# Optimization experiments

Measured on AMD Instinct MI355X. Metric: run time of the kernel, lower is better.

The kernel has to match this reference:

```python
import jax, jax.numpy as jnp
import numpy as np
import math

# Model dims (see shape_source)
BATCH, SEQ, HH, WW = 32, 128, 32, 32   # x: (B, seq_len, H, W); L = H*W = 1024
D_MODEL = 1024                          # hidden_dim
N2 = 4                                  # n=8 -> 4 complex S4D modes
L_MAX = 64                              # SSM kernel length (l_max)


def _layernorm(x, gamma, beta, eps=1e-5):
    mu = jnp.mean(x, axis=-1, keepdims=True)
    var = jnp.var(x, axis=-1, keepdims=True)
    return (x - mu) * jax.lax.rsqrt(var + eps) * gamma + beta


def setup_inputs() -> dict:
    key = jax.random.key(0)
    ks = jax.random.split(key, 12)
    d_in = SEQ  # d_input = d_output = seq_len
    inp = {
        "x": jax.random.normal(ks[0], (BATCH, SEQ, HH, WW), dtype=jnp.float32),
        # encoder Linear(d_input -> d_model)
        "W_enc": jax.random.normal(ks[1], (d_in, D_MODEL), dtype=jnp.float32) / math.sqrt(d_in),
        "b_enc": jnp.zeros((D_MODEL,), dtype=jnp.float32),
        # S4D SSM parameters (per d_model channel, N2 complex modes)
        "log_dt": (jax.random.uniform(ks[2], (D_MODEL,), dtype=jnp.float32)
                   * (math.log(0.1) - math.log(0.001)) + math.log(0.001)),
        "A_log_real": jnp.full((D_MODEL, N2), math.log(0.5), dtype=jnp.float32),
        "A_imag": jnp.broadcast_to(math.pi * jnp.arange(N2, dtype=jnp.float32), (D_MODEL, N2)).copy(),
        "C_real": jax.random.normal(ks[3], (D_MODEL, N2), dtype=jnp.float32) * 0.5,
        "C_imag": jax.random.normal(ks[4], (D_MODEL, N2), dtype=jnp.float32) * 0.5,
        "D": jax.random.normal(ks[5], (D_MODEL,), dtype=jnp.float32),
        # position-wise GLU mixing Linear(d_model -> 2*d_model)
        "W_glu": jax.random.normal(ks[6], (D_MODEL, 2 * D_MODEL), dtype=jnp.float32) / math.sqrt(D_MODEL),
        "b_glu": jnp.zeros((2 * D_MODEL,), dtype=jnp.float32),
        "ln_gamma": jnp.ones((D_MODEL,), dtype=jnp.float32),
        "ln_beta": jnp.zeros((D_MODEL,), dtype=jnp.float32),
        # decoder Linear(d_model -> d_output)
        "W_dec": jax.random.normal(ks[7], (D_MODEL, d_in), dtype=jnp.float32) / math.sqrt(D_MODEL),
        "b_dec": jnp.zeros((d_in,), dtype=jnp.float32),
    }
    return inp


def reference(x, W_enc, b_enc, log_dt, A_log_real, A_imag, C_real, C_imag, D,
              W_glu, b_glu, ln_gamma, ln_beta, W_dec, b_dec):
    Bsz, S, Hh, Ww = x.shape
    L = Hh * Ww
    u = x.reshape(Bsz, S, L)                                  # (B, d_input, L)
    # encoder applied per position along L
    h = jnp.einsum('bdl,de->ble', u, W_enc) + b_enc           # (B, L, d_model)

    # ---- S4D kernel (ZOH discretization, B=1, diagonal A) ----
    dt = jnp.exp(log_dt)                                      # (d,)
    A = -jnp.exp(A_log_real) + 1j * A_imag                    # (d, n2) complex
    Cc = C_real + 1j * C_imag
    dtA = A * dt[:, None]                                     # (d, n2)
    Bd = (jnp.exp(dtA) - 1.0) / A                             # ZOH input matrix
    t = jnp.arange(L_MAX)
    vand = jnp.exp(dtA[:, :, None] * t)                       # (d, n2, l_max)
    K = 2.0 * jnp.einsum('dn,dnl->dl', Cc * Bd, vand).real    # (d, l_max)

    # ---- causal FFT convolution along L + skip D*u ----
    z = jnp.swapaxes(h, 1, 2)                                 # (B, d, L)
    n_fft = L + L_MAX
    y = jnp.fft.irfft(jnp.fft.rfft(z, n=n_fft) * jnp.fft.rfft(K, n=n_fft), n=n_fft)[..., :L]
    y = y + D[:, None] * z                                    # (B, d, L)

    # ---- block: GELU -> GLU mixing -> residual -> LayerNorm ----
    y = jax.nn.gelu(jnp.swapaxes(y, 1, 2))                    # (B, L, d)
    g = y @ W_glu + b_glu                                     # (B, L, 2d)
    g = g[..., :D_MODEL] * jax.nn.sigmoid(g[..., D_MODEL:])
    h = _layernorm(h + g, ln_gamma, ln_beta)                  # (B, L, d)

    out = h @ W_dec + b_dec                                   # (B, L, d_output)
    out = jnp.swapaxes(out, 1, 2).reshape(Bsz, S, Hh, Ww)
    return out
```

## Files before the change

### kernel.cpp

```cpp
#include <hip/hip_runtime.h>
#include <hip/hip_bf16.h>
#include <math.h>

#define B_ 32
#define S_ 128
#define L_ 1024
#define D_ 1024

typedef unsigned short u16;
typedef __attribute__((ext_vector_type(8))) __bf16 bf16x8;
typedef __attribute__((ext_vector_type(4))) float f32x4;

__device__ __forceinline__ float bf2f(u16 u) {
    return __uint_as_float(((unsigned)u) << 16);
}
__device__ __forceinline__ u16 f2bf(float f) {
    unsigned u = __float_as_uint(f);
    u += 0x7FFF + ((u >> 16) & 1);
    return (u16)(u >> 16);
}
__device__ __forceinline__ float gelu_tanh(float x) {
    float x3 = x * x * x;
    float t = tanhf(0.7978845608028654f * (x + 0.044715f * x3));
    return 0.5f * x * (1.0f + t);
}
__device__ __forceinline__ float sigmoidf(float x) {
    return 1.0f / (1.0f + expf(-x));
}
__device__ __forceinline__ void gld16(const void* g, void* l) {
    __builtin_amdgcn_global_load_lds((const __attribute__((address_space(1))) void*)g,
                                     (__attribute__((address_space(3))) void*)l, 16, 0, 0);
}

__global__ __launch_bounds__(256) void k_ssmk(
        const float* __restrict__ log_dt, const float* __restrict__ Alr,
        const float* __restrict__ Aim, const float* __restrict__ Cr,
        const float* __restrict__ Ci, float* __restrict__ Kt) {
    int tid = blockIdx.x * 256 + threadIdx.x;
    int d = tid & (D_ - 1);
    int j = tid >> 10;
    float dt = expf(log_dt[d]);
    float acc = 0.f;
    #pragma unroll
    for (int n = 0; n < 4; ++n) {
        float ar = -expf(Alr[d * 4 + n]);
        float ai = Aim[d * 4 + n];
        float wr = ar * dt, wi = ai * dt;
        float ew = expf(wr);
        float sw, cw; sincosf(wi, &sw, &cw);
        float ur = ew * cw - 1.0f, ui = ew * sw;
        float inv = 1.0f / (ar * ar + ai * ai);
        float bdr = (ur * ar + ui * ai) * inv;
        float bdi = (ui * ar - ur * ai) * inv;
        float cr = Cr[d * 4 + n], ci = Ci[d * 4 + n];
        float cbr = cr * bdr - ci * bdi;
        float cbi = cr * bdi + ci * bdr;
        float ej = expf(wr * (float)j);
        float sj, cj; sincosf(wi * (float)j, &sj, &cj);
        acc += 2.0f * ej * (cbr * cj - cbi * sj);
    }
    Kt[j * D_ + d] = acc;
}

__global__ __launch_bounds__(256) void k_tcast(
        const float* __restrict__ src0, u16* __restrict__ dst0, int R, int C) {
    __shared__ float tile[64][65];
    const float* src = src0 + (size_t)blockIdx.z * R * C;
    u16* dst = dst0 + (size_t)blockIdx.z * R * C;
    int c0 = blockIdx.x * 64;
    int r0 = blockIdx.y * 64;
    int t = threadIdx.x;
    #pragma unroll
    for (int p = 0; p < 4; ++p) {
        int fid = p * 256 + t;
        int rr = fid >> 4, cc = (fid & 15) * 4;
        float4 v = *(const float4*)&src[(size_t)(r0 + rr) * C + c0 + cc];
        tile[rr][cc + 0] = v.x; tile[rr][cc + 1] = v.y;
        tile[rr][cc + 2] = v.z; tile[rr][cc + 3] = v.w;
    }
    __syncthreads();
    #pragma unroll
    for (int p = 0; p < 4; ++p) {
        int fid = p * 256 + t;
        int rr = fid >> 4, cc = (fid & 15) * 4;
        ushort4 o;
        o.x = f2bf(tile[cc + 0][rr]);
        o.y = f2bf(tile[cc + 1][rr]);
        o.z = f2bf(tile[cc + 2][rr]);
        o.w = f2bf(tile[cc + 3][rr]);
        *(ushort4*)&dst[(size_t)(c0 + rr) * R + r0 + cc] = o;
    }
}

__global__ __launch_bounds__(256) void k_enc_mfma(
        const u16* __restrict__ xb, const u16* __restrict__ WeT,
        const float* __restrict__ be, u16* __restrict__ hb) {
    __shared__ u16 As[128 * 128];
    __shared__ u16 Bs[128 * 128];
    int t = threadIdx.x;
    int lane = t & 63, wid = t >> 6;
    int wr = wid & 1, wc = wid >> 1;
    int orig = blockIdx.x;
    int wgid = (orig & 7) * 256 + (orig >> 3);
    int m0 = (wgid >> 3) * 128;
    int e0 = (wgid & 7) * 128;

    #pragma unroll
    for (int c = 0; c < 8; ++c) {
        int ch = wid * 8 + c;
        int r = ch * 4 + (lane >> 4);
        int g = (lane & 15) ^ (r & 15);
        gld16(&xb[(size_t)(m0 + r) * 128 + g * 8], &As[ch * 512]);
        gld16(&WeT[(size_t)(e0 + r) * 128 + g * 8], &Bs[ch * 512]);
    }
    int co4[4];
    #pragma unroll
    for (int kh = 0; kh < 4; ++kh)
        co4[kh] = ((((lane >> 4) + kh * 4) ^ (lane & 15)) * 8);
    int arow[4], brow[4];
    #pragma unroll
    for (int i = 0; i < 4; ++i) arow[i] = (wr * 64 + i * 16 + (lane & 15)) * 128;
    #pragma unroll
    for (int q = 0; q < 4; ++q) brow[q] = (wc * 64 + q * 16 + (lane & 15)) * 128;

    __syncthreads();
    f32x4 acc[4][4] = {};
    #pragma unroll
    for (int kh = 0; kh < 4; ++kh) {
        bf16x8 af[4], bfr[4];
        #pragma unroll
        for (int i = 0; i < 4; ++i) af[i] = *(const bf16x8*)&As[arow[i] + co4[kh]];
        #pragma unroll
        for (int q = 0; q < 4; ++q) bfr[q] = *(const bf16x8*)&Bs[brow[q] + co4[kh]];
        __builtin_amdgcn_s_setprio(1);
        #pragma unroll
        for (int i = 0; i < 4; ++i)
            #pragma unroll
            for (int q = 0; q < 4; ++q)
                acc[i][q] = __builtin_amdgcn_mfma_f32_16x16x32_bf16(af[i], bfr[q], acc[i][q], 0, 0, 0);
        __builtin_amdgcn_s_setprio(0);
    }
    #pragma unroll
    for (int q = 0; q < 4; ++q) {
        int e = e0 + wc * 64 + q * 16 + (lane & 15);
        float bias = be[e];
        #pragma unroll
        for (int i = 0; i < 4; ++i) {
            #pragma unroll
            for (int r = 0; r < 4; ++r) {
                int m = m0 + wr * 64 + i * 16 + (lane >> 4) * 4 + r;
                hb[(size_t)m * 1024 + e] = f2bf(acc[i][q][r] + bias);
            }
        }
    }
}

__global__ __launch_bounds__(256) void k_conv(
        const u16* __restrict__ hb, const float* __restrict__ Kt,
        const float* __restrict__ Dv, u16* __restrict__ yg) {
    __shared__ float hs[128][64];
    int b = blockIdx.z;
    int l0 = blockIdx.y * 64;
    int d0 = blockIdx.x * 64;
    int t = threadIdx.x;
    int dl = t & 63, lg = t >> 6;
    #pragma unroll
    for (int p = 0; p < 8; ++p) {
        int fid = p * 256 + t;
        int r = fid >> 4, c4 = fid & 15;
        int l = l0 - 64 + r;
        float4 v = make_float4(0.f, 0.f, 0.f, 0.f);
        if (l >= 0) {
            ushort4 u = *(const ushort4*)&hb[((size_t)b * 1024 + l) * 1024 + d0 + c4 * 4];
            v = make_float4(bf2f(u.x), bf2f(u.y), bf2f(u.z), bf2f(u.w));
        }
        *(float4*)&hs[r][c4 * 4] = v;
    }
    float kr[64];
    #pragma unroll
    for (int j = 0; j < 64; ++j) kr[j] = Kt[j * 1024 + d0 + dl];
    float Dd = Dv[d0 + dl];
    __syncthreads();
    float acc[16] = {};
    int rbase = lg * 16 + 1;
    #pragma unroll
    for (int s = 0; s < 15; ++s) {
        float hv = hs[rbase + s][dl];
        #pragma unroll
        for (int i = 0; i <= 14; ++i)
            if (i <= s) acc[i] = fmaf(kr[i + 63 - s], hv, acc[i]);
    }
    #pragma unroll
    for (int s = 15; s < 64; ++s) {
        float hv = hs[rbase + s][dl];
        #pragma unroll
        for (int i = 0; i < 16; ++i)
            acc[i] = fmaf(kr[i + 63 - s], hv, acc[i]);
    }
    #pragma unroll
    for (int s = 64; s < 79; ++s) {
        float hv = hs[rbase + s][dl];
        #pragma unroll
        for (int i = 1; i < 16; ++i)
            if (i >= s - 63) acc[i] = fmaf(kr[i + 63 - s], hv, acc[i]);
    }
    #pragma unroll
    for (int i = 0; i < 16; ++i) {
        int l = l0 + lg * 16 + i;
        float z = hs[64 + lg * 16 + i][dl];
        float y = acc[i] + Dd * z;
        yg[((size_t)b * 1024 + l) * 1024 + d0 + dl] = f2bf(gelu_tanh(y));
    }
}

__global__ __launch_bounds__(512, 2) void k_glu256(
        const u16* __restrict__ yg, const u16* __restrict__ WgT,
        const float* __restrict__ bg, u16* __restrict__ hb) {
    __shared__ u16 Asm[4][8192];
    __shared__ u16 Bsm[4][8192];
    int t = threadIdx.x;
    int lane = t & 63, wid = t >> 6;
    int wr = wid >> 2, wc = wid & 3;

    int orig = blockIdx.x;
    int wgid = (orig & 7) * 128 + (orig >> 3);
    int m0 = (wgid >> 3) * 256;
    int p0g = (wgid & 7) * 128;

    int crow = lane >> 2;
    int gofs = (((lane & 3) ^ ((lane >> 3) & 3)) * 8);
    int ch0 = wid * 2, ch1 = ch0 + 1;
    int rA0 = ch0 * 16 + crow, rA1 = ch1 * 16 + crow;
    int dA0 = ch0 * 512, dA1 = ch1 * 512;
    int gB0 = ((rA0 >> 4) & 1) * 1024 + p0g + (((rA0 >> 5) << 4) | (rA0 & 15));
    int gB1 = ((rA1 >> 4) & 1) * 1024 + p0g + (((rA1 >> 5) << 4) | (rA1 & 15));

    int aco = (lane & 15) * 32 + (((lane >> 4) ^ (((lane & 15) >> 1) & 3)) * 8);
    int abase = wr * 128 * 32;
    int bbase = wc * 64 * 32;

#define STAGE_A(T) { int k0_ = (T) * 32; u16* d_ = &Asm[(T) & 3][0]; \
    gld16(&yg[(size_t)(m0 + rA0) * 1024 + k0_ + gofs], d_ + dA0); \
    gld16(&yg[(size_t)(m0 + rA1) * 1024 + k0_ + gofs], d_ + dA1); }
#define STAGE_B(T) { int k0_ = (T) * 32; u16* d_ = &Bsm[(T) & 3][0]; \
    gld16(&WgT[(size_t)gB0 * 1024 + k0_ + gofs], d_ + dA0); \
    gld16(&WgT[(size_t)gB1 * 1024 + k0_ + gofs], d_ + dA1); }

    f32x4 acc[8][4] = {};
    bf16x8 af[4], bf[4];

    STAGE_A(0); STAGE_B(0); STAGE_A(1); STAGE_B(1); STAGE_A(2); STAGE_B(2);

#define TILE_BODY(KT, WAITN, DO_STAGE) { \
    asm volatile("s_waitcnt vmcnt(" #WAITN ")" ::: "memory"); \
    __builtin_amdgcn_s_barrier(); \
    __builtin_amdgcn_sched_barrier(0); \
    const u16* Ac_ = &Asm[(KT) & 3][0]; \
    const u16* Bc_ = &Bsm[(KT) & 3][0]; \
    _Pragma("unroll") for (int q = 0; q < 4; ++q) bf[q] = *(const bf16x8*)&Bc_[bbase + q * 512 + aco]; \
    _Pragma("unroll") for (int i = 0; i < 4; ++i) af[i] = *(const bf16x8*)&Ac_[abase + i * 512 + aco]; \
    if (DO_STAGE) STAGE_A((KT) + 3); \
    __builtin_amdgcn_s_setprio(1); \
    _Pragma("unroll") for (int i = 0; i < 4; ++i) \
        _Pragma("unroll") for (int q = 0; q < 4; ++q) \
            acc[i][q] = __builtin_amdgcn_mfma_f32_16x16x32_bf16(af[i], bf[q], acc[i][q], 0, 0, 0); \
    __builtin_amdgcn_s_setprio(0); \
    _Pragma("unroll") for (int i = 0; i < 4; ++i) af[i] = *(const bf16x8*)&Ac_[abase + 2048 + i * 512 + aco]; \
    if (DO_STAGE) STAGE_B((KT) + 3); \
    __builtin_amdgcn_s_setprio(1); \
    _Pragma("unroll") for (int i = 0; i < 4; ++i) \
        _Pragma("unroll") for (int q = 0; q < 4; ++q) \
            acc[4 + i][q] = __builtin_amdgcn_mfma_f32_16x16x32_bf16(af[i], bf[q], acc[4 + i][q], 0, 0, 0); \
    __builtin_amdgcn_s_setprio(0); }

    for (int kt = 0; kt < 29; ++kt) TILE_BODY(kt, 8, 1);
    TILE_BODY(29, 8, 0);
    TILE_BODY(30, 4, 0);
    TILE_BODY(31, 0, 0);
#undef TILE_BODY
#undef STAGE_A
#undef STAGE_B

    #pragma unroll
    for (int i = 0; i < 8; ++i) {
        #pragma unroll
        for (int tt = 0; tt < 2; ++tt) {
            int col = p0g + (wc * 2 + tt) * 16 + (lane & 15);
            float b1v = bg[col];
            float b2v = bg[1024 + col];
            #pragma unroll
            for (int r = 0; r < 4; ++r) {
                int m = m0 + wr * 128 + i * 16 + (lane >> 4) * 4 + r;
                size_t idx = (size_t)m * 1024 + col;
                float g1 = acc[i][tt * 2][r] + b1v;
                float g2 = acc[i][tt * 2 + 1][r] + b2v;
                hb[idx] = f2bf(bf2f(hb[idx]) + g1 * sigmoidf(g2));
            }
        }
    }
}

__global__ __launch_bounds__(256) void k_ln(
        u16* __restrict__ hb, const float* __restrict__ gamma,
        const float* __restrict__ beta) {
    int row = blockIdx.x;
    int t = threadIdx.x;
    size_t base = (size_t)row * 1024;
    ushort4 u = *(const ushort4*)&hb[base + t * 4];
    float v0 = bf2f(u.x), v1 = bf2f(u.y), v2 = bf2f(u.z), v3 = bf2f(u.w);
    float s = v0 + v1 + v2 + v3;
    float s2 = v0 * v0 + v1 * v1 + v2 * v2 + v3 * v3;
    #pragma unroll
    for (int off = 32; off > 0; off >>= 1) {
        s += __shfl_down(s, off);
        s2 += __shfl_down(s2, off);
    }
    __shared__ float rs[4], rs2[4];
    int wid = t >> 6, lane = t & 63;
    if (lane == 0) { rs[wid] = s; rs2[wid] = s2; }
    __syncthreads();
    float ts = rs[0] + rs[1] + rs[2] + rs[3];
    float ts2 = rs2[0] + rs2[1] + rs2[2] + rs2[3];
    float mean = ts * (1.0f / 1024.0f);
    float var = ts2 * (1.0f / 1024.0f) - mean * mean;
    float rstd = rsqrtf(var + 1e-5f);
    float4 gm = *(const float4*)&gamma[t * 4];
    float4 bt = *(const float4*)&beta[t * 4];
    ushort4 o;
    o.x = f2bf((v0 - mean) * rstd * gm.x + bt.x);
    o.y = f2bf((v1 - mean) * rstd * gm.y + bt.y);
    o.z = f2bf((v2 - mean) * rstd * gm.z + bt.z);
    o.w = f2bf((v3 - mean) * rstd * gm.w + bt.w);
    *(ushort4*)&hb[base + t * 4] = o;
}

__global__ __launch_bounds__(256) void k_dec_mfma(
        const u16* __restrict__ hb, const u16* __restrict__ WdT,
        const float* __restrict__ bd, float* __restrict__ out) {
    __shared__ __align__(16) char smem[65536];
    u16* As = (u16*)smem;
    u16* Bs = (u16*)(smem + 32768);
    float* Ts = (float*)smem;
    int t = threadIdx.x;
    int lane = t & 63, wid = t >> 6;
    int wr = wid & 1, wc = wid >> 1;
    int m0 = blockIdx.x * 128;
    int bb = m0 >> 10, l0 = m0 & 1023;

    int gsrc = (((lane & 7) ^ (lane >> 3)) * 8);
    int rr4[4];
    #pragma unroll
    for (int c = 0; c < 4; ++c) rr4[c] = (wid * 4 + c) * 8 + (lane >> 3);
    int co[2];
    co[0] = (((lane >> 4) + 0) ^ (lane & 7)) * 8;
    co[1] = (((lane >> 4) + 4) ^ (lane & 7)) * 8;
    int arow[4], brow[4];
    #pragma unroll
    for (int i = 0; i < 4; ++i) arow[i] = (wr * 64 + i * 16 + (lane & 15)) * 64;
    #pragma unroll
    for (int q = 0; q < 4; ++q) brow[q] = (wc * 64 + q * 16 + (lane & 15)) * 64;

    f32x4 acc[4][4] = {};
    #pragma unroll
    for (int c = 0; c < 4; ++c) {
        int ch = wid * 4 + c;
        gld16(&hb[(size_t)(m0 + rr4[c]) * 1024 + gsrc], &As[0 * 8192 + ch * 512]);
        gld16(&WdT[(size_t)rr4[c] * 1024 + gsrc], &Bs[0 * 8192 + ch * 512]);
    }
    __syncthreads();
    int cur = 0;
    for (int kt = 0; kt < 16; ++kt) {
        if (kt < 15) {
            int k0 = (kt + 1) * 64;
            #pragma unroll
            for (int c = 0; c < 4; ++c) {
                int ch = wid * 4 + c;
                gld16(&hb[(size_t)(m0 + rr4[c]) * 1024 + k0 + gsrc], &As[(cur ^ 1) * 8192 + ch * 512]);
                gld16(&WdT[(size_t)rr4[c] * 1024 + k0 + gsrc], &Bs[(cur ^ 1) * 8192 + ch * 512]);
            }
        }
        #pragma unroll
        for (int kh = 0; kh < 2; ++kh) {
            bf16x8 af[4], bfr[4];
            #pragma unroll
            for (int i = 0; i < 4; ++i) af[i] = *(const bf16x8*)&As[cur * 8192 + arow[i] + co[kh]];
            #pragma unroll
            for (int q = 0; q < 4; ++q) bfr[q] = *(const bf16x8*)&Bs[cur * 8192 + brow[q] + co[kh]];
            __builtin_amdgcn_s_setprio(1);
            #pragma unroll
            for (int i = 0; i < 4; ++i)
                #pragma unroll
                for (int q = 0; q < 4; ++q)
                    acc[i][q] = __builtin_amdgcn_mfma_f32_16x16x32_bf16(af[i], bfr[q], acc[i][q], 0, 0, 0);
            __builtin_amdgcn_s_setprio(0);
        }
        __syncthreads();
        cur ^= 1;
    }
    __syncthreads();
    #pragma unroll
    for (int ro = 0; ro < 2; ++ro) {
        if (wc == ro) {
            #pragma unroll
            for (int i = 0; i < 4; ++i)
                #pragma unroll
                for (int q = 0; q < 4; ++q) {
                    int sl = q * 16 + (lane & 15);
                    float bias = bd[ro * 64 + sl];
                    #pragma unroll
                    for (int r = 0; r < 4; ++r) {
                        int ml = wr * 64 + i * 16 + (lane >> 4) * 4 + r;
                        Ts[sl * 132 + ml] = acc[i][q][r] + bias;
                    }
                }
        }
        __syncthreads();
        #pragma unroll
        for (int p = 0; p < 8; ++p) {
            int fid = p * 256 + t;
            int sl = fid >> 5, c = (fid & 31) * 4;
            float4 v = *(const float4*)&Ts[sl * 132 + c];
            *(float4*)&out[(size_t)bb * 131072 + (size_t)(ro * 64 + sl) * 1024 + l0 + c] = v;
        }
        __syncthreads();
    }
}

extern "C" void kernel_launch(void* const* d_in, const int* in_sizes, int n_in,
                              void* d_out, int out_size, void* d_ws, size_t ws_size,
                              hipStream_t stream) {
    (void)in_sizes; (void)n_in; (void)out_size; (void)ws_size;
    const float* x   = (const float*)d_in[0];
    const float* We  = (const float*)d_in[1];
    const float* be  = (const float*)d_in[2];
    const float* ldt = (const float*)d_in[3];
    const float* Alr = (const float*)d_in[4];
    const float* Aim = (const float*)d_in[5];
    const float* Cr  = (const float*)d_in[6];
    const float* Ci  = (const float*)d_in[7];
    const float* Dv  = (const float*)d_in[8];
    const float* Wg  = (const float*)d_in[9];
    const float* bg  = (const float*)d_in[10];
    const float* gam = (const float*)d_in[11];
    const float* bet = (const float*)d_in[12];
    const float* Wd  = (const float*)d_in[13];
    const float* bd  = (const float*)d_in[14];
    float* out = (float*)d_out;

    u16* hb = (u16*)d_ws;
    u16* yg = hb + 33554432ull;
    float* Kt = (float*)(yg + 33554432ull);
    u16* WgT = (u16*)(Kt + 65536);
    u16* WdT = WgT + 2097152ull;
    u16* WeT = WdT + 131072ull;
    u16* xb  = yg;

    k_tcast<<<dim3(32, 16, 1), 256, 0, stream>>>(Wg, WgT, 1024, 2048);
    k_tcast<<<dim3(2, 16, 1), 256, 0, stream>>>(Wd, WdT, 1024, 128);
    k_tcast<<<dim3(16, 2, 1), 256, 0, stream>>>(We, WeT, 128, 1024);
    k_tcast<<<dim3(16, 2, 32), 256, 0, stream>>>(x, xb, 128, 1024);
    k_ssmk<<<256, 256, 0, stream>>>(ldt, Alr, Aim, Cr, Ci, Kt);
    k_enc_mfma<<<2048, 256, 0, stream>>>(xb, WeT, be, hb);
    k_conv<<<dim3(16, 16, 32), 256, 0, stream>>>(hb, Kt, Dv, yg);
    k_glu256<<<1024, 512, 0, stream>>>(yg, WgT, bg, hb);
    k_ln<<<32768, 256, 0, stream>>>(hb, gam, bet);
    k_dec_mfma<<<256, 256, 0, stream>>>(hb, WdT, bd, out);
}
```

Before: 349.6 us.

## Restructure GLU GEMM into 64-wide K tiles with four-phase double-buffered pipeline

Result: no change. 348.6 us (-0.3%).

```diff
diff --git a/kernel.cpp b/kernel.cpp
--- a/kernel.cpp
+++ b/kernel.cpp
@@ -216,8 +216,7 @@
 __global__ __launch_bounds__(512, 2) void k_glu256(
         const u16* __restrict__ yg, const u16* __restrict__ WgT,
         const float* __restrict__ bg, u16* __restrict__ hb) {
-    __shared__ u16 Asm[4][8192];
-    __shared__ u16 Bsm[4][8192];
+    __shared__ u16 S[65536];
     int t = threadIdx.x;
     int lane = t & 63, wid = t >> 6;
     int wr = wid >> 2, wc = wid & 3;
@@ -227,73 +226,104 @@
     int m0 = (wgid >> 3) * 256;
     int p0g = (wgid & 7) * 128;
 
-    int crow = lane >> 2;
-    int gofs = (((lane & 3) ^ ((lane >> 3) & 3)) * 8);
+    int gofs = (((lane & 7) ^ ((lane >> 3) & 7)) * 8);
     int ch0 = wid * 2, ch1 = ch0 + 1;
-    int rA0 = ch0 * 16 + crow, rA1 = ch1 * 16 + crow;
-    int dA0 = ch0 * 512, dA1 = ch1 * 512;
-    int gB0 = ((rA0 >> 4) & 1) * 1024 + p0g + (((rA0 >> 5) << 4) | (rA0 & 15));
-    int gB1 = ((rA1 >> 4) & 1) * 1024 + p0g + (((rA1 >> 5) << 4) | (rA1 & 15));
-
-    int aco = (lane & 15) * 32 + (((lane >> 4) ^ (((lane & 15) >> 1) & 3)) * 8);
-    int abase = wr * 128 * 32;
-    int bbase = wc * 64 * 32;
-
-#define STAGE_A(T) { int k0_ = (T) * 32; u16* d_ = &Asm[(T) & 3][0]; \
-    gld16(&yg[(size_t)(m0 + rA0) * 1024 + k0_ + gofs], d_ + dA0); \
-    gld16(&yg[(size_t)(m0 + rA1) * 1024 + k0_ + gofs], d_ + dA1); }
-#define STAGE_B(T) { int k0_ = (T) * 32; u16* d_ = &Bsm[(T) & 3][0]; \
-    gld16(&WgT[(size_t)gB0 * 1024 + k0_ + gofs], d_ + dA0); \
-    gld16(&WgT[(size_t)gB1 * 1024 + k0_ + gofs], d_ + dA1); }
-
-    f32x4 acc[8][4] = {};
-    bf16x8 af[4], bf[4];
-
-    STAGE_A(0); STAGE_B(0); STAGE_A(1); STAGE_B(1); STAGE_A(2); STAGE_B(2);
-
-#define TILE_BODY(KT, WAITN, DO_STAGE) { \
-    asm volatile("s_waitcnt vmcnt(" #WAITN ")" ::: "memory"); \
-    __builtin_amdgcn_s_barrier(); \
-    __builtin_amdgcn_sched_barrier(0); \
-    const u16* Ac_ = &Asm[(KT) & 3][0]; \
-    const u16* Bc_ = &Bsm[(KT) & 3][0]; \
-    _Pragma("unroll") for (int q = 0; q < 4; ++q) bf[q] = *(const bf16x8*)&Bc_[bbase + q * 512 + aco]; \
-    _Pragma("unroll") for (int i = 0; i < 4; ++i) af[i] = *(const bf16x8*)&Ac_[abase + i * 512 + aco]; \
-    if (DO_STAGE) STAGE_A((KT) + 3); \
+    int dst0 = ch0 * 512 + lane * 8;
+    int dst1 = ch1 * 512 + lane * 8;
+    int gmA[2][2], gmB[2][2];
+    #pragma unroll
+    for (int h = 0; h < 2; ++h) {
+        #pragma unroll
+        for (int j = 0; j < 2; ++j) {
+            int ch = ch0 + j;
+            gmA[h][j] = m0 + (ch >> 3) * 128 + h * 64 + (ch & 7) * 8 + (lane >> 3);
+            int r = (ch >> 2) * 64 + h * 32 + (ch & 3) * 8 + (lane >> 3);
+            gmB[h][j] = ((r >> 4) & 1) * 1024 + p0g + (((r >> 5) << 4) | (r & 15));
+        }
+    }
+    int co[2];
+    co[0] = (((lane >> 4) + 0) ^ (lane & 7)) * 8;
+    co[1] = (((lane >> 4) + 4) ^ (lane & 7)) * 8;
+    int arow[4], brow[2];
+    #pragma unroll
+    for (int i = 0; i < 4; ++i) arow[i] = (wr * 64 + i * 16 + (lane & 15)) * 64;
+    #pragma unroll
+    for (int q = 0; q < 2; ++q) brow[q] = (wc * 32 + q * 16 + (lane & 15)) * 64;
+
+#define GLD_A(H, BUF, K0) { u16* d_ = &S[((BUF) * 2 + (H)) * 8192]; \
+    gld16(&yg[(size_t)gmA[H][0] * 1024 + (K0) + gofs], d_ + dst0); \
+    gld16(&yg[(size_t)gmA[H][1] * 1024 + (K0) + gofs], d_ + dst1); }
+#define GLD_B(H, BUF, K0) { u16* d_ = &S[32768 + ((BUF) * 2 + (H)) * 8192]; \
+    gld16(&WgT[(size_t)gmB[H][0] * 1024 + (K0) + gofs], d_ + dst0); \
+    gld16(&WgT[(size_t)gmB[H][1] * 1024 + (K0) + gofs], d_ + dst1); }
+
+#define PHASE(MS, NS, STAGE_STMT) { \
+    const u16* Ar_ = &S[(cbuf * 2 + (MS)) * 8192]; \
+    const u16* Br_ = &S[32768 + (cbuf * 2 + (NS)) * 8192]; \
+    bf16x8 a_[4][2], b_[2][2]; \
+    _Pragma("unroll") for (int q = 0; q < 2; ++q) { \
+        b_[q][0] = *(const bf16x8*)&Br_[brow[q] + co[0]]; \
+        b_[q][1] = *(const bf16x8*)&Br_[brow[q] + co[1]]; } \
+    _Pragma("unroll") for (int i = 0; i < 4; ++i) { \
+        a_[i][0] = *(const bf16x8*)&Ar_[arow[i] + co[0]]; \
+        a_[i][1] = *(const bf16x8*)&Ar_[arow[i] + co[1]]; } \
+    STAGE_STMT; \
     __builtin_amdgcn_s_setprio(1); \
     _Pragma("unroll") for (int i = 0; i < 4; ++i) \
-        _Pragma("unroll") for (int q = 0; q < 4; ++q) \
-            acc[i][q] = __builtin_amdgcn_mfma_f32_16x16x32_bf16(af[i], bf[q], acc[i][q], 0, 0, 0); \
-    __builtin_amdgcn_s_setprio(0); \
-    _Pragma("unroll") for (int i = 0; i < 4; ++i) af[i] = *(const bf16x8*)&Ac_[abase + 2048 + i * 512 + aco]; \
-    if (DO_STAGE) STAGE_B((KT) + 3); \
-    __builtin_amdgcn_s_setprio(1); \
-    _Pragma("unroll") for (int i = 0; i < 4; ++i) \
-        _Pragma("unroll") for (int q = 0; q < 4; ++q) \
-            acc[4 + i][q] = __builtin_amdgcn_mfma_f32_16x16x32_bf16(af[i], bf[q], acc[4 + i][q], 0, 0, 0); \
+        _Pragma("unroll") for (int q = 0; q < 2; ++q) { \
+            acc[(MS) * 4 + i][(NS) * 2 + q] = __builtin_amdgcn_mfma_f32_16x16x32_bf16( \
+                a_[i][0], b_[q][0], acc[(MS) * 4 + i][(NS) * 2 + q], 0, 0, 0); \
+            acc[(MS) * 4 + i][(NS) * 2 + q] = __builtin_amdgcn_mfma_f32_16x16x32_bf16( \
+                a_[i][1], b_[q][1], acc[(MS) * 4 + i][(NS) * 2 + q], 0, 0, 0); } \
     __builtin_amdgcn_s_setprio(0); }
 
-    for (int kt = 0; kt < 29; ++kt) TILE_BODY(kt, 8, 1);
-    TILE_BODY(29, 8, 0);
-    TILE_BODY(30, 4, 0);
-    TILE_BODY(31, 0, 0);
-#undef TILE_BODY
-#undef STAGE_A
-#undef STAGE_B
+#define BAR() { __builtin_amdgcn_s_barrier(); __builtin_amdgcn_sched_barrier(0); }
+
+    f32x4 acc[8][4] = {};
+
+    GLD_A(0, 0, 0); GLD_B(0, 0, 0); GLD_B(1, 0, 0); GLD_A(1, 0, 0);
+    GLD_A(0, 1, 64); GLD_B(0, 1, 64);
+
+    for (int kt = 0; kt < 15; ++kt) {
+        int cbuf = kt & 1, nbuf = cbuf ^ 1;
+        int k1 = (kt + 1) * 64, k2 = (kt + 2) * 64;
+        asm volatile("s_waitcnt vmcnt(4)" ::: "memory");
+        BAR();
+        PHASE(0, 0, { GLD_B(1, nbuf, k1); });
+        BAR();
+        PHASE(0, 1, { GLD_A(1, nbuf, k1); });
+        BAR();
+        PHASE(1, 0, { if (kt < 14) GLD_A(0, cbuf, k2); });
+        BAR();
+        PHASE(1, 1, { if (kt < 14) GLD_B(0, cbuf, k2); });
+    }
+    {
+        int cbuf = 1;
+        asm volatile("s_waitcnt vmcnt(0)" ::: "memory");
+        BAR();
+        PHASE(0, 0, {});
+        PHASE(0, 1, {});
+        PHASE(1, 0, {});
+        PHASE(1, 1, {});
+    }
+#undef GLD_A
+#undef GLD_B
+#undef PHASE
+#undef BAR
 
     #pragma unroll
     for (int i = 0; i < 8; ++i) {
         #pragma unroll
-        for (int tt = 0; tt < 2; ++tt) {
-            int col = p0g + (wc * 2 + tt) * 16 + (lane & 15);
+        for (int pb = 0; pb < 2; ++pb) {
+            int col = p0g + (wc * 2 + pb) * 16 + (lane & 15);
             float b1v = bg[col];
             float b2v = bg[1024 + col];
             #pragma unroll
             for (int r = 0; r < 4; ++r) {
                 int m = m0 + wr * 128 + i * 16 + (lane >> 4) * 4 + r;
                 size_t idx = (size_t)m * 1024 + col;
-                float g1 = acc[i][tt * 2][r] + b1v;
-                float g2 = acc[i][tt * 2 + 1][r] + b2v;
+                float g1 = acc[i][pb * 2][r] + b1v;
+                float g2 = acc[i][pb * 2 + 1][r] + b2v;
                 hb[idx] = f2bf(bf2f(hb[idx]) + g1 * sigmoidf(g2));
             }
         }
```
